# Kernel tuning notes

Measured on AMD Instinct MI355X. Metric: run time of the kernel, lower is better.

The kernel has to match this reference:

```python
import jax, jax.numpy as jnp
import numpy as np

RADIUS = 8.0   # matches init kwarg radius
EPS = 1e-8     # nn.CosineSimilarity eps


def _denorm(p, height, width):
    # kornia denormalize_pixel_coordinates: [-1,1] -> [0, size-1]
    scale = jnp.array([(width - 1) * 0.5, (height - 1) * 0.5], dtype=p.dtype)
    return (p + 1.0) * scale


def setup_inputs() -> dict:
    key = jax.random.key(0)
    k1, k2, k3, k4 = jax.random.split(key, 4)
    B, N, D = 4, 2048, 256
    features = jax.random.normal(k1, (B, N, D), dtype=jnp.float32)
    pts_src = jax.random.uniform(k2, (B, N, 2), dtype=jnp.float32) * 2.0 - 1.0
    pts_dst = jax.random.uniform(k3, (B, B, N, 2), dtype=jnp.float32) * 2.0 - 1.0
    invis_idx = jax.random.randint(k4, (3, 128), 0, N)
    return {"features": features, "pts_src": pts_src, "pts_dst": pts_dst,
            "invis_idx": invis_idx, "height": 480, "width": 640}


def reference(features, pts_src, pts_dst, invis_idx, height, width):
    # features: [B,N,D]; pts_src: [B,N,2]; pts_dst: [B,B,N,2]
    B, N, D = features.shape
    ps = _denorm(jax.lax.stop_gradient(pts_src), height, width)   # [B,N,2]
    pd = _denorm(jax.lax.stop_gradient(pts_dst), height, width)   # [B,B,N,2]

    # squared euclidean distance d2[i,j,n,m] = ||ps[i,n] - pd[i,j,m]||^2
    s_src = jnp.sum(ps * ps, axis=-1)          # [B,N]
    s_dst = jnp.sum(pd * pd, axis=-1)          # [B,B,N]
    cross = jnp.einsum('ind,ijmd->ijnm', ps, pd)
    d2 = s_src[:, None, :, None] + s_dst[:, :, None, :] - 2.0 * cross  # [B,B,N,N]
    mask = d2 <= RADIUS * RADIUS

    # pair p = i*B + j of the flattened [B^2] grid matches src batch j (p % B)
    # with dst batch i (p // B):
    # cos[i,j,n,m] = <features[j,n], features[i,m]> / max(|f_jn|*|f_im|, eps)
    dots = jnp.einsum('jnd,imd->ijnm', features, features)  # [B,B,N,N]
    norms = jnp.sqrt(jnp.sum(features * features, axis=-1))  # [B,N]
    denom = jnp.maximum(norms[None, :, :, None] * norms[:, None, None, :], EPS)
    cos = dots / denom

    cnt = jnp.maximum(jnp.sum(mask), 1).astype(features.dtype)
    return jnp.sum(jnp.where(mask, 1.0 - cos, 0.0)) / cnt
```

## Files before the change

### kernel.cpp

```cpp
#include <hip/hip_runtime.h>

#define BB 4
#define NN 2048
#define DD 256
#define TILE_N 32
#define NPW 8
#define NT (NN / TILE_N)
#define MSPLIT 2
#define MLEN (NN / MSPLIT)
#define MCH (MLEN / 128)
#define WQ_CAP 96
#define NBLK (BB * BB * NT * MSPLIT)

__global__ __launch_bounds__(256) void scan_kernel(const float* __restrict__ feat,
                                                   const float* __restrict__ pts_src,
                                                   const float* __restrict__ pts_dst,
                                                   const int* __restrict__ hptr,
                                                   const int* __restrict__ wptr,
                                                   float* __restrict__ psum,
                                                   unsigned int* __restrict__ pcnt) {
    __shared__ unsigned int wq[4][WQ_CAP];
    __shared__ unsigned int wqc[4];
    __shared__ float bsum[4];
    __shared__ unsigned int bcnt[4];
    const int pair  = blockIdx.x >> 7;
    const int tile  = (blockIdx.x >> 1) & (NT - 1);
    const int mhalf = blockIdx.x & 1;
    const int mbase = mhalf * MLEN;
    const int i = pair >> 2;
    const int j = pair & 3;
    const float sx = ((float)(*wptr) - 1.0f) * 0.5f;
    const float sy = ((float)(*hptr) - 1.0f) * 0.5f;

    const int wave = threadIdx.x >> 6;
    const int lane = threadIdx.x & 63;
    if (lane == 0) wqc[wave] = 0u;

    const int nbase = tile * TILE_N + wave * NPW;
    float psx[NPW], psy[NPW];
#pragma unroll
    for (int k = 0; k < NPW; ++k) {
        psx[k] = fmaf(pts_src[(size_t)(i * NN + nbase + k) * 2 + 0], sx, sx);
        psy[k] = fmaf(pts_src[(size_t)(i * NN + nbase + k) * 2 + 1], sy, sy);
    }

    const float4* pd = (const float4*)(pts_dst + (size_t)pair * NN * 2 + (size_t)mbase * 2);

    float4 q = pd[lane];
#pragma unroll
    for (int c = 0; c < MCH; ++c) {
        float4 qn;
        if (c + 1 < MCH) qn = pd[(c + 1) * 64 + lane];
        const float qx0 = fmaf(q.x, sx, sx), qy0 = fmaf(q.y, sy, sy);
        const float qx1 = fmaf(q.z, sx, sx), qy1 = fmaf(q.w, sy, sy);
        float mn = 1e30f;
#pragma unroll
        for (int k = 0; k < NPW; ++k) {
            const float ax = psx[k] - qx0, ay = psy[k] - qy0;
            const float bx = psx[k] - qx1, by = psy[k] - qy1;
            mn = fminf(mn, fminf(fmaf(ax, ax, ay * ay), fmaf(bx, bx, by * by)));
        }
        if (__ballot(mn <= 64.0f)) {
            const unsigned int m2 = (unsigned int)(mbase + c * 128 + 2 * lane);
#pragma unroll
            for (int k = 0; k < NPW; ++k) {
                const float ax = psx[k] - qx0, ay = psy[k] - qy0;
                const float bx = psx[k] - qx1, by = psy[k] - qy1;
                const float d0 = fmaf(ax, ax, ay * ay);
                const float d1 = fmaf(bx, bx, by * by);
                if (fminf(d0, d1) <= 64.0f) {
                    if (d0 <= 64.0f) {
                        const unsigned int slot = atomicAdd(&wqc[wave], 1u);
                        if (slot < WQ_CAP) wq[wave][slot] = ((unsigned int)k << 11) | m2;
                    }
                    if (d1 <= 64.0f) {
                        const unsigned int slot = atomicAdd(&wqc[wave], 1u);
                        if (slot < WQ_CAP) wq[wave][slot] = ((unsigned int)k << 11) | (m2 + 1u);
                    }
                }
            }
        }
        q = qn;
    }

    const unsigned int hc = min(wqc[wave], (unsigned int)WQ_CAP);
    const int g = lane >> 2, sub = lane & 3;
    float lsum = 0.0f;
    for (unsigned int h0 = 0; h0 < hc; h0 += 16) {
        const unsigned int hid = h0 + (unsigned int)g;
        const bool valid = hid < hc;
        float dd = 0.0f, aa = 0.0f, bb = 0.0f;
        if (valid) {
            const unsigned int rec = wq[wave][hid];
            const int m = (int)(rec & 2047u);
            const int n = nbase + (int)(rec >> 11);
            const float4* pa = (const float4*)(feat + (size_t)(j * NN + n) * DD);
            const float4* pb = (const float4*)(feat + (size_t)(i * NN + m) * DD);
#pragma unroll
            for (int t = 0; t < 16; ++t) {
                const float4 a = pa[t * 4 + sub];
                const float4 b = pb[t * 4 + sub];
                dd = fmaf(a.x, b.x, fmaf(a.y, b.y, fmaf(a.z, b.z, fmaf(a.w, b.w, dd))));
                aa = fmaf(a.x, a.x, fmaf(a.y, a.y, fmaf(a.z, a.z, fmaf(a.w, a.w, aa))));
                bb = fmaf(b.x, b.x, fmaf(b.y, b.y, fmaf(b.z, b.z, fmaf(b.w, b.w, bb))));
            }
        }
        dd += __shfl_xor(dd, 1, 64);  aa += __shfl_xor(aa, 1, 64);  bb += __shfl_xor(bb, 1, 64);
        dd += __shfl_xor(dd, 2, 64);  aa += __shfl_xor(aa, 2, 64);  bb += __shfl_xor(bb, 2, 64);
        if (valid && sub == 0) {
            const float p = aa * bb;
            float r = rsqrtf(p);
            r = r * (1.5f - 0.5f * p * r * r);
            lsum += 1.0f - dd * r;
        }
    }
#pragma unroll
    for (int off = 32; off >= 1; off >>= 1) lsum += __shfl_xor(lsum, off, 64);

    if (lane == 0) { bsum[wave] = lsum; bcnt[wave] = hc; }
    __syncthreads();
    if (threadIdx.x == 0) {
        psum[blockIdx.x] = bsum[0] + bsum[1] + bsum[2] + bsum[3];
        pcnt[blockIdx.x] = bcnt[0] + bcnt[1] + bcnt[2] + bcnt[3];
    }
}

__global__ __launch_bounds__(256) void finalize_kernel(const float* __restrict__ psum,
                                                       const unsigned int* __restrict__ pcnt,
                                                       float* __restrict__ out) {
    float s = 0.0f;
    float c = 0.0f;
    for (int t = threadIdx.x; t < NBLK; t += 256) {
        s += psum[t];
        c += (float)pcnt[t];
    }
#pragma unroll
    for (int off = 32; off >= 1; off >>= 1) {
        s += __shfl_xor(s, off, 64);
        c += __shfl_xor(c, off, 64);
    }
    __shared__ float ss[4], cc[4];
    const int wave = threadIdx.x >> 6;
    const int lane = threadIdx.x & 63;
    if (lane == 0) { ss[wave] = s; cc[wave] = c; }
    __syncthreads();
    if (threadIdx.x == 0) {
        const float S = ss[0] + ss[1] + ss[2] + ss[3];
        const float C = cc[0] + cc[1] + cc[2] + cc[3];
        out[0] = S / fmaxf(C, 1.0f);
    }
}

extern "C" void kernel_launch(void* const* d_in, const int* in_sizes, int n_in,
                              void* d_out, int out_size, void* d_ws, size_t ws_size,
                              hipStream_t stream) {
    const float* feat    = (const float*)d_in[0];
    const float* pts_src = (const float*)d_in[1];
    const float* pts_dst = (const float*)d_in[2];
    const int* hptr = (const int*)d_in[4];
    const int* wptr = (const int*)d_in[5];
    float* out = (float*)d_out;

    float*        psum  = (float*)d_ws;
    unsigned int* pcnt  = (unsigned int*)((char*)d_ws + 8192);

    scan_kernel<<<NBLK, 256, 0, stream>>>(feat, pts_src, pts_dst,
                                          hptr, wptr, psum, pcnt);
    finalize_kernel<<<1, 256, 0, stream>>>(psum, pcnt, out);
}
```

Measured before the change: 86.95 us.

## Prenormalize features into fp16 buffer and use half-precision dot products

Adds a pack kernel that L2-normalizes each feature row and stores it as fp16 in workspace. The scan kernel then gathers half-size rows and computes only the dot product, dropping the per-pair norm accumulation and rsqrt. This halves gather bandwidth and removes redundant norm work, but it adds an extra kernel launch plus a full pass over the features, and it loses precision through fp16 rounding.

```diff
diff --git a/kernel.cpp b/kernel.cpp
--- a/kernel.cpp
+++ b/kernel.cpp
@@ -1,4 +1,5 @@
 #include <hip/hip_runtime.h>
+#include <hip/hip_fp16.h>
 
 #define BB 4
 #define NN 2048
@@ -12,7 +13,23 @@
 #define WQ_CAP 96
 #define NBLK (BB * BB * NT * MSPLIT)
 
-__global__ __launch_bounds__(256) void scan_kernel(const float* __restrict__ feat,
+__global__ __launch_bounds__(256) void pack_kernel(const float* __restrict__ feat,
+                                                   __half* __restrict__ fh) {
+    const int wave = threadIdx.x >> 6;
+    const int lane = threadIdx.x & 63;
+    const int row  = blockIdx.x * 4 + wave;
+    const float4 v = ((const float4*)(feat + (size_t)row * DD))[lane];
+    float s = fmaf(v.x, v.x, fmaf(v.y, v.y, fmaf(v.z, v.z, v.w * v.w)));
+#pragma unroll
+    for (int off = 32; off >= 1; off >>= 1) s += __shfl_xor(s, off, 64);
+    float rn = rsqrtf(s);
+    rn = rn * (1.5f - 0.5f * s * rn * rn);
+    __half2* dst = (__half2*)(fh + (size_t)row * DD);
+    dst[2 * lane + 0] = __floats2half2_rn(v.x * rn, v.y * rn);
+    dst[2 * lane + 1] = __floats2half2_rn(v.z * rn, v.w * rn);
+}
+
+__global__ __launch_bounds__(256) void scan_kernel(const __half* __restrict__ fh,
                                                    const float* __restrict__ pts_src,
                                                    const float* __restrict__ pts_dst,
                                                    const int* __restrict__ hptr,
@@ -89,30 +106,30 @@
     for (unsigned int h0 = 0; h0 < hc; h0 += 16) {
         const unsigned int hid = h0 + (unsigned int)g;
         const bool valid = hid < hc;
-        float dd = 0.0f, aa = 0.0f, bb = 0.0f;
+        float dd = 0.0f;
         if (valid) {
             const unsigned int rec = wq[wave][hid];
             const int m = (int)(rec & 2047u);
             const int n = nbase + (int)(rec >> 11);
-            const float4* pa = (const float4*)(feat + (size_t)(j * NN + n) * DD);
-            const float4* pb = (const float4*)(feat + (size_t)(i * NN + m) * DD);
+            const float4* pa = (const float4*)(fh + (size_t)(j * NN + n) * DD);
+            const float4* pb = (const float4*)(fh + (size_t)(i * NN + m) * DD);
 #pragma unroll
-            for (int t = 0; t < 16; ++t) {
-                const float4 a = pa[t * 4 + sub];
-                const float4 b = pb[t * 4 + sub];
-                dd = fmaf(a.x, b.x, fmaf(a.y, b.y, fmaf(a.z, b.z, fmaf(a.w, b.w, dd))));
-                aa = fmaf(a.x, a.x, fmaf(a.y, a.y, fmaf(a.z, a.z, fmaf(a.w, a.w, aa))));
-                bb = fmaf(b.x, b.x, fmaf(b.y, b.y, fmaf(b.z, b.z, fmaf(b.w, b.w, bb))));
+            for (int t = 0; t < 8; ++t) {
+                const float4 A = pa[t * 4 + sub];
+                const float4 B = pb[t * 4 + sub];
+                const __half2* ah = (const __half2*)&A;
+                const __half2* bh = (const __half2*)&B;
+#pragma unroll
+                for (int u = 0; u < 4; ++u) {
+                    const float2 fa2 = __half22float2(ah[u]);
+                    const float2 fb2 = __half22float2(bh[u]);
+                    dd = fmaf(fa2.x, fb2.x, fmaf(fa2.y, fb2.y, dd));
+                }
             }
         }
-        dd += __shfl_xor(dd, 1, 64);  aa += __shfl_xor(aa, 1, 64);  bb += __shfl_xor(bb, 1, 64);
-        dd += __shfl_xor(dd, 2, 64);  aa += __shfl_xor(aa, 2, 64);  bb += __shfl_xor(bb, 2, 64);
-        if (valid && sub == 0) {
-            const float p = aa * bb;
-            float r = rsqrtf(p);
-            r = r * (1.5f - 0.5f * p * r * r);
-            lsum += 1.0f - dd * r;
-        }
+        dd += __shfl_xor(dd, 1, 64);
+        dd += __shfl_xor(dd, 2, 64);
+        if (valid && sub == 0) lsum += 1.0f - dd;
     }
 #pragma unroll
     for (int off = 32; off >= 1; off >>= 1) lsum += __shfl_xor(lsum, off, 64);
@@ -161,10 +178,12 @@
     const int* wptr = (const int*)d_in[5];
     float* out = (float*)d_out;
 
-    float*        psum  = (float*)d_ws;
-    unsigned int* pcnt  = (unsigned int*)((char*)d_ws + 8192);
+    float*        psum = (float*)d_ws;
+    unsigned int* pcnt = (unsigned int*)((char*)d_ws + 8192);
+    __half*       fh   = (__half*)((char*)d_ws + 65536);
 
-    scan_kernel<<<NBLK, 256, 0, stream>>>(feat, pts_src, pts_dst,
+    pack_kernel<<<BB * NN / 4, 256, 0, stream>>>(feat, fh);
+    scan_kernel<<<NBLK, 256, 0, stream>>>(fh, pts_src, pts_dst,
                                           hptr, wptr, psum, pcnt);
     finalize_kernel<<<1, 256, 0, stream>>>(psum, pcnt, out);
 }
```

Measured after the change: 87.32 us. About the same (+0.4%).

## Bin destination points into x-strips to prune radius search

Applied to the files above, without the earlier changes.

Adds a pre-pass kernel that sorts each pair's destination points into 16-pixel-wide x-strips using counting sort in shared memory, storing the sorted positions and original indices. The scan kernel then visits only the strips within ±8 pixels of each source point instead of brute-force testing all 2048 destination points. The MSPLIT split along m is dropped, halving the number of scan blocks. This costs an extra kernel launch and workspace traffic, and the per-source-point loop is serialized across k with variable trip counts.

```diff
diff --git a/kernel.cpp b/kernel.cpp
--- a/kernel.cpp
+++ b/kernel.cpp
@@ -6,15 +6,61 @@
 #define TILE_N 32
 #define NPW 8
 #define NT (NN / TILE_N)
-#define MSPLIT 2
-#define MLEN (NN / MSPLIT)
-#define MCH (MLEN / 128)
+#define NPAIR (BB * BB)
+#define NBLK (NPAIR * NT)
 #define WQ_CAP 96
-#define NBLK (BB * BB * NT * MSPLIT)
+#define MAXC 64
+
+
+__global__ __launch_bounds__(256) void bin_kernel(const float* __restrict__ pts_dst,
+                                                  const int* __restrict__ hptr,
+                                                  const int* __restrict__ wptr,
+                                                  float2* __restrict__ pos2,
+                                                  unsigned int* __restrict__ sidx,
+                                                  unsigned int* __restrict__ sstart) {
+    __shared__ unsigned int cnt[MAXC];
+    __shared__ unsigned int off[MAXC];
+    __shared__ unsigned int cur[MAXC];
+    const int pair = blockIdx.x;
+    const int tid = threadIdx.x;
+    const float sx = ((float)(*wptr) - 1.0f) * 0.5f;
+    const float sy = ((float)(*hptr) - 1.0f) * 0.5f;
+    const int ncell = min(MAXC - 1, ((*wptr - 1) >> 4) + 1);
+    if (tid < MAXC) cnt[tid] = 0u;
+    __syncthreads();
+    float px[8], py[8];
+    int pc[8];
+    const float2* src = (const float2*)(pts_dst) + (size_t)pair * NN;
+#pragma unroll
+    for (int r = 0; r < 8; ++r) {
+        const float2 p = src[r * 256 + tid];
+        px[r] = fmaf(p.x, sx, sx);
+        py[r] = fmaf(p.y, sy, sy);
+        pc[r] = min(ncell - 1, max(0, (int)(px[r] * 0.0625f)));
+        atomicAdd(&cnt[pc[r]], 1u);
+    }
+    __syncthreads();
+    if (tid == 0) {
+        unsigned int run = 0u;
+        for (int c = 0; c < ncell; ++c) { off[c] = run; cur[c] = run; run += cnt[c]; }
+        for (int c = ncell; c < MAXC; ++c) off[c] = run;
+    }
+    __syncthreads();
+#pragma unroll
+    for (int r = 0; r < 8; ++r) {
+        const unsigned int slot = atomicAdd(&cur[pc[r]], 1u);
+        pos2[(size_t)pair * NN + slot] = make_float2(px[r], py[r]);
+        sidx[(size_t)pair * NN + slot] = (unsigned int)(r * 256 + tid);
+    }
+    __syncthreads();
+    if (tid < MAXC) sstart[pair * MAXC + tid] = off[tid];
+}
 
 __global__ __launch_bounds__(256) void scan_kernel(const float* __restrict__ feat,
                                                    const float* __restrict__ pts_src,
-                                                   const float* __restrict__ pts_dst,
+                                                   const float2* __restrict__ pos2,
+                                                   const unsigned int* __restrict__ sidx,
+                                                   const unsigned int* __restrict__ sstart,
                                                    const int* __restrict__ hptr,
                                                    const int* __restrict__ wptr,
                                                    float* __restrict__ psum,
@@ -23,64 +69,51 @@
     __shared__ unsigned int wqc[4];
     __shared__ float bsum[4];
     __shared__ unsigned int bcnt[4];
-    const int pair  = blockIdx.x >> 7;
-    const int tile  = (blockIdx.x >> 1) & (NT - 1);
-    const int mhalf = blockIdx.x & 1;
-    const int mbase = mhalf * MLEN;
+    const int pair = blockIdx.x >> 6;
+    const int tile = blockIdx.x & (NT - 1);
     const int i = pair >> 2;
     const int j = pair & 3;
     const float sx = ((float)(*wptr) - 1.0f) * 0.5f;
     const float sy = ((float)(*hptr) - 1.0f) * 0.5f;
+    const int ncell = min(MAXC - 1, ((*wptr - 1) >> 4) + 1);
 
     const int wave = threadIdx.x >> 6;
     const int lane = threadIdx.x & 63;
     if (lane == 0) wqc[wave] = 0u;
 
     const int nbase = tile * TILE_N + wave * NPW;
+    const float2* ppos = pos2 + (size_t)pair * NN;
+    const unsigned int* pidx = sidx + (size_t)pair * NN;
+
     float psx[NPW], psy[NPW];
+    int b0[NPW], e1[NPW];
 #pragma unroll
     for (int k = 0; k < NPW; ++k) {
         psx[k] = fmaf(pts_src[(size_t)(i * NN + nbase + k) * 2 + 0], sx, sx);
         psy[k] = fmaf(pts_src[(size_t)(i * NN + nbase + k) * 2 + 1], sy, sy);
-    }
-
-    const float4* pd = (const float4*)(pts_dst + (size_t)pair * NN * 2 + (size_t)mbase * 2);
-
-    float4 q = pd[lane];
-#pragma unroll
-    for (int c = 0; c < MCH; ++c) {
-        float4 qn;
-        if (c + 1 < MCH) qn = pd[(c + 1) * 64 + lane];
-        const float qx0 = fmaf(q.x, sx, sx), qy0 = fmaf(q.y, sy, sy);
-        const float qx1 = fmaf(q.z, sx, sx), qy1 = fmaf(q.w, sy, sy);
-        float mn = 1e30f;
-#pragma unroll
-        for (int k = 0; k < NPW; ++k) {
-            const float ax = psx[k] - qx0, ay = psy[k] - qy0;
-            const float bx = psx[k] - qx1, by = psy[k] - qy1;
-            mn = fminf(mn, fminf(fmaf(ax, ax, ay * ay), fmaf(bx, bx, by * by)));
-        }
-        if (__ballot(mn <= 64.0f)) {
-            const unsigned int m2 = (unsigned int)(mbase + c * 128 + 2 * lane);
-#pragma unroll
-            for (int k = 0; k < NPW; ++k) {
-                const float ax = psx[k] - qx0, ay = psy[k] - qy0;
-                const float bx = psx[k] - qx1, by = psy[k] - qy1;
-                const float d0 = fmaf(ax, ax, ay * ay);
-                const float d1 = fmaf(bx, bx, by * by);
-                if (fminf(d0, d1) <= 64.0f) {
-                    if (d0 <= 64.0f) {
-                        const unsigned int slot = atomicAdd(&wqc[wave], 1u);
-                        if (slot < WQ_CAP) wq[wave][slot] = ((unsigned int)k << 11) | m2;
-                    }
-                    if (d1 <= 64.0f) {
-                        const unsigned int slot = atomicAdd(&wqc[wave], 1u);
-                        if (slot < WQ_CAP) wq[wave][slot] = ((unsigned int)k << 11) | (m2 + 1u);
-                    }
+        const int c0 = max(0, (int)((psx[k] - 8.0f) * 0.0625f));
+        const int c1 = min(ncell - 1, (int)((psx[k] + 8.0f) * 0.0625f));
+        b0[k] = (int)sstart[pair * MAXC + c0];
+        e1[k] = (int)sstart[pair * MAXC + c1 + 1];
+    }
+
+#pragma unroll 1
+    for (int k = 0; k < NPW; ++k) {
+        for (int base = b0[k]; base < e1[k]; base += 64) {
+            const int t = base + lane;
+            const bool in = t < e1[k];
+            const float2 p = ppos[in ? t : base];
+            const float ax = psx[k] - p.x;
+            const float ay = psy[k] - p.y;
+            const bool hit = in && (fmaf(ax, ax, ay * ay) <= 64.0f);
+            if (__ballot(hit)) {
+                if (hit) {
+                    const unsigned int slot = atomicAdd(&wqc[wave], 1u);
+                    if (slot < WQ_CAP)
+                        wq[wave][slot] = ((unsigned int)k << 11) | pidx[t];
                 }
             }
         }
-        q = qn;
     }
 
     const unsigned int hc = min(wqc[wave], (unsigned int)WQ_CAP);
@@ -161,10 +194,14 @@
     const int* wptr = (const int*)d_in[5];
     float* out = (float*)d_out;
 
-    float*        psum  = (float*)d_ws;
-    unsigned int* pcnt  = (unsigned int*)((char*)d_ws + 8192);
-
-    scan_kernel<<<NBLK, 256, 0, stream>>>(feat, pts_src, pts_dst,
+    float*        psum   = (float*)d_ws;
+    unsigned int* pcnt   = (unsigned int*)((char*)d_ws + 4096);
+    unsigned int* sstart = (unsigned int*)((char*)d_ws + 8192);
+    unsigned int* sidx   = (unsigned int*)((char*)d_ws + 16384);
+    float2*       pos2   = (float2*)((char*)d_ws + 262144);
+
+    bin_kernel<<<NPAIR, 256, 0, stream>>>(pts_dst, hptr, wptr, pos2, sidx, sstart);
+    scan_kernel<<<NBLK, 256, 0, stream>>>(feat, pts_src, pos2, sidx, sstart,
                                           hptr, wptr, psum, pcnt);
     finalize_kernel<<<1, 256, 0, stream>>>(psum, pcnt, out);
 }
```

Result: slower. 93.97 us (+8.1%).
